# Kernel optimization log

Measured on AMD Instinct MI355X. Metric: run time of the kernel, lower is better.

The kernel has to match this reference:

```python
import jax, jax.numpy as jnp
import numpy as np

N = 20000        # nodes
E = 320000       # edges (avg degree 16)
IN = 128         # in_channels
D = 64           # out_channels == per-head dim (PyG TransformerConv)
H = 4            # heads
EPS_BN = 1e-5


def setup_inputs() -> dict:
    key = jax.random.key(0)
    ks = jax.random.split(key, 12)
    x = jax.random.normal(ks[0], (N, IN), jnp.float32)
    edge_index = jax.random.randint(ks[1], (2, E), 0, N, dtype=jnp.int64)
    s = 1.0 / np.sqrt(IN)
    Wq = jax.random.normal(ks[2], (IN, H * D), jnp.float32) * s
    bq = jnp.zeros((H * D,), jnp.float32)
    Wk = jax.random.normal(ks[3], (IN, H * D), jnp.float32) * s
    bk = jnp.zeros((H * D,), jnp.float32)
    Wv = jax.random.normal(ks[4], (IN, H * D), jnp.float32) * s
    bv = jnp.zeros((H * D,), jnp.float32)
    Wskip = jax.random.normal(ks[5], (IN, D), jnp.float32) * s
    bskip = jnp.zeros((D,), jnp.float32)
    gamma = jnp.ones((D,), jnp.float32)
    beta = jnp.zeros((D,), jnp.float32)
    return {"x": x, "edge_index": edge_index, "Wq": Wq, "bq": bq,
            "Wk": Wk, "bk": bk, "Wv": Wv, "bv": bv,
            "Wskip": Wskip, "bskip": bskip, "gamma": gamma, "beta": beta}


def reference(x, edge_index, Wq, bq, Wk, bk, Wv, bv, Wskip, bskip, gamma, beta):
    src = edge_index[0]   # message source j
    dst = edge_index[1]   # message target i
    # node-level projections, [N, H, D]
    q = (x @ Wq + bq).reshape(N, H, D)
    k = (x @ Wk + bk).reshape(N, H, D)
    v = (x @ Wv + bv).reshape(N, H, D)
    # per-edge attention logits [E, H]
    scores = jnp.einsum('ehd,ehd->eh', q[dst], k[src]) / jnp.sqrt(jnp.float32(D))
    # segment softmax over incoming edges of each target node
    smax = jax.ops.segment_max(scores, dst, num_segments=N)
    smax = jnp.where(jnp.isfinite(smax), smax, 0.0)  # isolated nodes
    p = jnp.exp(scores - smax[dst])
    denom = jax.ops.segment_sum(p, dst, num_segments=N)
    alpha = p / (denom[dst] + 1e-16)                  # [E, H]
    # scatter-aggregate messages: [N, H, D]
    msg = jax.ops.segment_sum(alpha[:, :, None] * v[src], dst, num_segments=N)
    # concat=False -> mean over heads; root skip connection
    out = msg.mean(axis=1) + x @ Wskip + bskip        # [N, D]
    # BatchNorm1d over nodes (training-mode batch stats, biased var)
    mu = out.mean(axis=0)
    var = out.var(axis=0)
    out = (out - mu) * jax.lax.rsqrt(var + EPS_BN) * gamma + beta
    # exact (erf) GELU, dropout = identity at eval
    return jax.nn.gelu(out, approximate=False)
```

## Files before the change

### kernel.cpp

```cpp
#include <hip/hip_runtime.h>
#include <math.h>

#define NNODES 20000
#define NEDGES 320000
#define CIN 128
#define DOUT 64
#define NHEAD 4
#define HD 256
#define PROJW 832

__global__ __launch_bounds__(256) void proj_kernel(
    const float* __restrict__ x,
    const float* __restrict__ Wq, const float* __restrict__ bq,
    const float* __restrict__ Wk, const float* __restrict__ bk,
    const float* __restrict__ Wv, const float* __restrict__ bv,
    const float* __restrict__ Ws, const float* __restrict__ bs,
    float* __restrict__ proj)
{
    __shared__ float Ast[32][68];
    __shared__ float Bs[32][68];
    const int tile_n = blockIdx.x;
    const float* W; const float* bias; int segw; int lc0;
    if (tile_n < 4)       { W = Wq; bias = bq; segw = HD;   lc0 = tile_n * 64; }
    else if (tile_n < 8)  { W = Wk; bias = bk; segw = HD;   lc0 = (tile_n - 4) * 64; }
    else if (tile_n < 12) { W = Wv; bias = bv; segw = HD;   lc0 = (tile_n - 8) * 64; }
    else                  { W = Ws; bias = bs; segw = DOUT; lc0 = 0; }
    const int row0 = blockIdx.y * 64;
    const int tid = threadIdx.x;
    const int tx = tid & 15, ty = tid >> 4;

    float acc[4][4] = {};
    for (int k0 = 0; k0 < CIN; k0 += 32) {
        #pragma unroll
        for (int l = 0; l < 2; ++l) {
            int idx = tid + l * 256;
            int r = idx >> 3, c4 = (idx & 7) << 2;
            int gr = row0 + r;
            float4 v = make_float4(0.f, 0.f, 0.f, 0.f);
            if (gr < NNODES)
                v = *reinterpret_cast<const float4*>(x + (size_t)gr * CIN + k0 + c4);
            Ast[c4 + 0][r] = v.x; Ast[c4 + 1][r] = v.y;
            Ast[c4 + 2][r] = v.z; Ast[c4 + 3][r] = v.w;
        }
        #pragma unroll
        for (int l = 0; l < 2; ++l) {
            int idx = tid + l * 256;
            int r = idx >> 4, c4 = (idx & 15) << 2;
            float4 v = *reinterpret_cast<const float4*>(W + (size_t)(k0 + r) * segw + lc0 + c4);
            *reinterpret_cast<float4*>(&Bs[r][c4]) = v;
        }
        __syncthreads();
        #pragma unroll
        for (int kk = 0; kk < 32; ++kk) {
            const float4 a = *reinterpret_cast<const float4*>(&Ast[kk][ty * 4]);
            const float4 b = *reinterpret_cast<const float4*>(&Bs[kk][tx * 4]);
            acc[0][0] += a.x * b.x; acc[0][1] += a.x * b.y; acc[0][2] += a.x * b.z; acc[0][3] += a.x * b.w;
            acc[1][0] += a.y * b.x; acc[1][1] += a.y * b.y; acc[1][2] += a.y * b.z; acc[1][3] += a.y * b.w;
            acc[2][0] += a.z * b.x; acc[2][1] += a.z * b.y; acc[2][2] += a.z * b.z; acc[2][3] += a.z * b.w;
            acc[3][0] += a.w * b.x; acc[3][1] += a.w * b.y; acc[3][2] += a.w * b.z; acc[3][3] += a.w * b.w;
        }
        __syncthreads();
    }
    const int colg0 = tile_n * 64;
    #pragma unroll
    for (int i = 0; i < 4; ++i) {
        int gr = row0 + ty * 4 + i;
        if (gr < NNODES) {
            float4 o;
            o.x = acc[i][0] + bias[lc0 + tx * 4 + 0];
            o.y = acc[i][1] + bias[lc0 + tx * 4 + 1];
            o.z = acc[i][2] + bias[lc0 + tx * 4 + 2];
            o.w = acc[i][3] + bias[lc0 + tx * 4 + 3];
            *reinterpret_cast<float4*>(proj + (size_t)gr * PROJW + colg0 + tx * 4) = o;
        }
    }
}

__global__ void hist_kernel(const int* __restrict__ ei, int* __restrict__ deg)
{
    int e = blockIdx.x * blockDim.x + threadIdx.x;
    if (e >= NEDGES) return;
    atomicAdd(&deg[ei[NEDGES + e]], 1);
}

__global__ __launch_bounds__(1024) void scan_kernel(
    const int* __restrict__ deg, int* __restrict__ rowptr, int* __restrict__ cursor)
{
    __shared__ int sd[1024];
    const int t = threadIdx.x;
    const int chunk = 20;
    const int base = t * chunk;
    int tsum = 0;
    for (int i = 0; i < chunk; ++i) {
        int idx = base + i;
        tsum += (idx < NNODES) ? deg[idx] : 0;
    }
    sd[t] = tsum; __syncthreads();
    for (int off = 1; off < 1024; off <<= 1) {
        int v = (t >= off) ? sd[t - off] : 0;
        __syncthreads();
        sd[t] += v;
        __syncthreads();
    }
    int run = sd[t] - tsum;
    for (int i = 0; i < chunk; ++i) {
        int idx = base + i;
        if (idx < NNODES) {
            int d = deg[idx];
            rowptr[idx] = run; cursor[idx] = run;
            run += d;
        }
    }
    if (t == 1023) rowptr[NNODES] = sd[1023];
}

__global__ void scatter_kernel(const int* __restrict__ ei, int* __restrict__ cursor,
                               int* __restrict__ col)
{
    int e = blockIdx.x * blockDim.x + threadIdx.x;
    if (e >= NEDGES) return;
    int src = ei[e];
    int dst = ei[NEDGES + e];
    int pos = atomicAdd(&cursor[dst], 1);
    col[pos] = src;
}

__global__ __launch_bounds__(256) void attn_kernel(
    const float* __restrict__ proj,
    const int* __restrict__ rowptr, const int* __restrict__ col,
    float* __restrict__ out_pre)
{
    const int node = blockIdx.x * 4 + (threadIdx.x >> 6);
    if (node >= NNODES) return;
    const int lane = threadIdx.x & 63;
    const int lane4 = lane * 4;

    const size_t nb = (size_t)node * PROJW;
    const float4 q = *reinterpret_cast<const float4*>(proj + nb + lane4);

    float m = -INFINITY, l = 0.f;
    float ax = 0.f, ay = 0.f, az = 0.f, aw = 0.f;
    int p = rowptr[node];
    const int pend = rowptr[node + 1];

    int j = (p < pend) ? col[p] : 0;
    const float* bj = proj + (size_t)j * PROJW + lane4;
    float4 kv = *reinterpret_cast<const float4*>(bj + 256);
    float4 vv = *reinterpret_cast<const float4*>(bj + 512);

    for (; p < pend; ++p) {
        const int p1 = p + 1;
        const int jn = (p1 < pend) ? col[p1] : j;
        const float* bn = proj + (size_t)jn * PROJW + lane4;
        const float4 kvn = *reinterpret_cast<const float4*>(bn + 256);
        const float4 vvn = *reinterpret_cast<const float4*>(bn + 512);

        float partial = q.x * kv.x + q.y * kv.y + q.z * kv.z + q.w * kv.w;
        partial += __shfl_xor(partial, 1, 16);
        partial += __shfl_xor(partial, 2, 16);
        partial += __shfl_xor(partial, 4, 16);
        partial += __shfl_xor(partial, 8, 16);
        const float s = partial * 0.125f;
        const float mnew = fmaxf(m, s);
        const float scale = __expf(m - mnew);
        const float pc = __expf(s - mnew);
        l = l * scale + pc;
        ax = ax * scale + pc * vv.x;
        ay = ay * scale + pc * vv.y;
        az = az * scale + pc * vv.z;
        aw = aw * scale + pc * vv.w;
        m = mnew;
        kv = kvn; vv = vvn;
    }
    const float inv = 1.f / (l + 1e-16f);
    float rx = ax * inv, ry = ay * inv, rz = az * inv, rw = aw * inv;
    rx += __shfl_xor(rx, 16); rx += __shfl_xor(rx, 32);
    ry += __shfl_xor(ry, 16); ry += __shfl_xor(ry, 32);
    rz += __shfl_xor(rz, 16); rz += __shfl_xor(rz, 32);
    rw += __shfl_xor(rw, 16); rw += __shfl_xor(rw, 32);
    if (lane < 16) {
        const float4 sk = *reinterpret_cast<const float4*>(proj + nb + 768 + lane4);
        float4 o;
        o.x = rx * 0.25f + sk.x;
        o.y = ry * 0.25f + sk.y;
        o.z = rz * 0.25f + sk.z;
        o.w = rw * 0.25f + sk.w;
        *reinterpret_cast<float4*>(out_pre + (size_t)node * DOUT + lane4) = o;
    }
}

__global__ __launch_bounds__(256) void bnred_kernel(
    const float* __restrict__ out_pre, float* __restrict__ bnacc)
{
    const int tid = threadIdx.x;
    const int c = tid & 63, g = tid >> 6;
    float s = 0.f, ss = 0.f;
    for (int r = blockIdx.x * 4 + g; r < NNODES; r += gridDim.x * 4) {
        float v = out_pre[(size_t)r * DOUT + c];
        s += v; ss += v * v;
    }
    __shared__ float sd[256];
    sd[tid] = s; __syncthreads();
    float s4 = 0.f;
    if (g == 0) s4 = sd[tid] + sd[tid + 64] + sd[tid + 128] + sd[tid + 192];
    __syncthreads();
    sd[tid] = ss; __syncthreads();
    if (g == 0) {
        float ss4 = sd[tid] + sd[tid + 64] + sd[tid + 128] + sd[tid + 192];
        atomicAdd(&bnacc[c], s4);
        atomicAdd(&bnacc[64 + c], ss4);
    }
}

__global__ __launch_bounds__(256) void final_kernel(
    const float* __restrict__ out_pre, const float* __restrict__ bnacc,
    const float* __restrict__ gamma, const float* __restrict__ beta,
    float* __restrict__ out)
{
    int idx = blockIdx.x * blockDim.x + threadIdx.x;
    if (idx >= NNODES * DOUT) return;
    const int c = idx & 63;
    const float mu = bnacc[c] * (1.f / NNODES);
    const float var = bnacc[64 + c] * (1.f / NNODES) - mu * mu;
    float v = (out_pre[idx] - mu) * rsqrtf(var + 1e-5f) * gamma[c] + beta[c];
    out[idx] = v * 0.5f * (1.f + erff(v * 0.70710678118654752f));
}

extern "C" void kernel_launch(void* const* d_in, const int* in_sizes, int n_in,
                              void* d_out, int out_size, void* d_ws, size_t ws_size,
                              hipStream_t stream) {
    const float* x     = (const float*)d_in[0];
    const int*   ei    = (const int*)d_in[1];
    const float* Wq    = (const float*)d_in[2];
    const float* bq    = (const float*)d_in[3];
    const float* Wk    = (const float*)d_in[4];
    const float* bk    = (const float*)d_in[5];
    const float* Wv    = (const float*)d_in[6];
    const float* bv    = (const float*)d_in[7];
    const float* Wskip = (const float*)d_in[8];
    const float* bskip = (const float*)d_in[9];
    const float* gamma = (const float*)d_in[10];
    const float* beta  = (const float*)d_in[11];
    float* out = (float*)d_out;

    float* proj    = (float*)d_ws;
    float* out_pre = proj + (size_t)NNODES * PROJW;
    float* bnacc   = out_pre + (size_t)NNODES * DOUT;
    int*   deg     = (int*)(bnacc + 128);
    int*   rowptr  = deg + NNODES;
    int*   cursor  = rowptr + NNODES + 1;
    int*   col     = cursor + NNODES;

    hipMemsetAsync(bnacc, 0, (128 + NNODES) * sizeof(int), stream);

    proj_kernel<<<dim3(13, (NNODES + 63) / 64), 256, 0, stream>>>(
        x, Wq, bq, Wk, bk, Wv, bv, Wskip, bskip, proj);
    hist_kernel<<<(NEDGES + 255) / 256, 256, 0, stream>>>(ei, deg);
    scan_kernel<<<1, 1024, 0, stream>>>(deg, rowptr, cursor);
    scatter_kernel<<<(NEDGES + 255) / 256, 256, 0, stream>>>(ei, cursor, col);
    attn_kernel<<<NNODES / 4, 256, 0, stream>>>(proj, rowptr, col, out_pre);
    bnred_kernel<<<128, 256, 0, stream>>>(out_pre, bnacc);
    final_kernel<<<(NNODES * DOUT + 255) / 256, 256, 0, stream>>>(
        out_pre, bnacc, gamma, beta, out);
}
```

Baseline: 316.0 us.

## Store K/V projections in fp16 separate buffer to halve gather traffic

The projection kernel now writes K and V as half precision into a dedicated packed buffer, while Q and the skip projection stay fp32 in a narrower buffer. The attention kernel gathers the per-edge K/V rows as fp16 and converts them to float, halving the bytes moved in the edge gather, which is the dominant random-access cost. It also shrinks the write traffic of the projection. The cost is fp16 rounding of K and V, which adds a small accuracy loss in the attention scores and the aggregation.

After: 277.7 us. 12.1% less time.

```diff
diff --git a/kernel.cpp b/kernel.cpp
--- a/kernel.cpp
+++ b/kernel.cpp
@@ -1,4 +1,5 @@
 #include <hip/hip_runtime.h>
+#include <hip/hip_fp16.h>
 #include <math.h>
 
 #define NNODES 20000
@@ -7,7 +8,8 @@
 #define DOUT 64
 #define NHEAD 4
 #define HD 256
-#define PROJW 832
+#define PROJW 320
+#define KVW 512
 
 __global__ __launch_bounds__(256) void proj_kernel(
     const float* __restrict__ x,
@@ -15,7 +17,7 @@
     const float* __restrict__ Wk, const float* __restrict__ bk,
     const float* __restrict__ Wv, const float* __restrict__ bv,
     const float* __restrict__ Ws, const float* __restrict__ bs,
-    float* __restrict__ proj)
+    float* __restrict__ proj, __half* __restrict__ kvh)
 {
     __shared__ float Ast[32][68];
     __shared__ float Bs[32][68];
@@ -61,17 +63,26 @@
         }
         __syncthreads();
     }
-    const int colg0 = tile_n * 64;
     #pragma unroll
     for (int i = 0; i < 4; ++i) {
         int gr = row0 + ty * 4 + i;
-        if (gr < NNODES) {
-            float4 o;
-            o.x = acc[i][0] + bias[lc0 + tx * 4 + 0];
-            o.y = acc[i][1] + bias[lc0 + tx * 4 + 1];
-            o.z = acc[i][2] + bias[lc0 + tx * 4 + 2];
-            o.w = acc[i][3] + bias[lc0 + tx * 4 + 3];
-            *reinterpret_cast<float4*>(proj + (size_t)gr * PROJW + colg0 + tx * 4) = o;
+        if (gr >= NNODES) continue;
+        float4 o;
+        o.x = acc[i][0] + bias[lc0 + tx * 4 + 0];
+        o.y = acc[i][1] + bias[lc0 + tx * 4 + 1];
+        o.z = acc[i][2] + bias[lc0 + tx * 4 + 2];
+        o.w = acc[i][3] + bias[lc0 + tx * 4 + 3];
+        if (tile_n < 4) {
+            *reinterpret_cast<float4*>(proj + (size_t)gr * PROJW + tile_n * 64 + tx * 4) = o;
+        } else if (tile_n < 12) {
+            int col = (tile_n < 8) ? (tile_n - 4) * 64 + tx * 4
+                                   : 256 + (tile_n - 8) * 64 + tx * 4;
+            __half2 h0 = __floats2half2_rn(o.x, o.y);
+            __half2 h1 = __floats2half2_rn(o.z, o.w);
+            __half2* dst = reinterpret_cast<__half2*>(kvh + (size_t)gr * KVW + col);
+            dst[0] = h0; dst[1] = h1;
+        } else {
+            *reinterpret_cast<float4*>(proj + (size_t)gr * PROJW + 256 + tx * 4) = o;
         }
     }
 }
@@ -126,7 +137,7 @@
 }
 
 __global__ __launch_bounds__(256) void attn_kernel(
-    const float* __restrict__ proj,
+    const float* __restrict__ proj, const __half* __restrict__ kvh,
     const int* __restrict__ rowptr, const int* __restrict__ col,
     float* __restrict__ out_pre)
 {
@@ -135,8 +146,7 @@
     const int lane = threadIdx.x & 63;
     const int lane4 = lane * 4;
 
-    const size_t nb = (size_t)node * PROJW;
-    const float4 q = *reinterpret_cast<const float4*>(proj + nb + lane4);
+    const float4 q = *reinterpret_cast<const float4*>(proj + (size_t)node * PROJW + lane4);
 
     float m = -INFINITY, l = 0.f;
     float ax = 0.f, ay = 0.f, az = 0.f, aw = 0.f;
@@ -144,18 +154,20 @@
     const int pend = rowptr[node + 1];
 
     int j = (p < pend) ? col[p] : 0;
-    const float* bj = proj + (size_t)j * PROJW + lane4;
-    float4 kv = *reinterpret_cast<const float4*>(bj + 256);
-    float4 vv = *reinterpret_cast<const float4*>(bj + 512);
+    const __half* bj = kvh + (size_t)j * KVW + lane4;
+    uint2 kraw = *reinterpret_cast<const uint2*>(bj);
+    uint2 vraw = *reinterpret_cast<const uint2*>(bj + 256);
 
     for (; p < pend; ++p) {
         const int p1 = p + 1;
         const int jn = (p1 < pend) ? col[p1] : j;
-        const float* bn = proj + (size_t)jn * PROJW + lane4;
-        const float4 kvn = *reinterpret_cast<const float4*>(bn + 256);
-        const float4 vvn = *reinterpret_cast<const float4*>(bn + 512);
-
-        float partial = q.x * kv.x + q.y * kv.y + q.z * kv.z + q.w * kv.w;
+        const __half* bn = kvh + (size_t)jn * KVW + lane4;
+        const uint2 krawn = *reinterpret_cast<const uint2*>(bn);
+        const uint2 vrawn = *reinterpret_cast<const uint2*>(bn + 256);
+
+        const float2 k0 = __half22float2(*reinterpret_cast<const __half2*>(&kraw.x));
+        const float2 k1 = __half22float2(*reinterpret_cast<const __half2*>(&kraw.y));
+        float partial = q.x * k0.x + q.y * k0.y + q.z * k1.x + q.w * k1.y;
         partial += __shfl_xor(partial, 1, 16);
         partial += __shfl_xor(partial, 2, 16);
         partial += __shfl_xor(partial, 4, 16);
@@ -164,13 +176,15 @@
         const float mnew = fmaxf(m, s);
         const float scale = __expf(m - mnew);
         const float pc = __expf(s - mnew);
+        const float2 v0 = __half22float2(*reinterpret_cast<const __half2*>(&vraw.x));
+        const float2 v1 = __half22float2(*reinterpret_cast<const __half2*>(&vraw.y));
         l = l * scale + pc;
-        ax = ax * scale + pc * vv.x;
-        ay = ay * scale + pc * vv.y;
-        az = az * scale + pc * vv.z;
-        aw = aw * scale + pc * vv.w;
+        ax = ax * scale + pc * v0.x;
+        ay = ay * scale + pc * v0.y;
+        az = az * scale + pc * v1.x;
+        aw = aw * scale + pc * v1.y;
         m = mnew;
-        kv = kvn; vv = vvn;
+        kraw = krawn; vraw = vrawn;
     }
     const float inv = 1.f / (l + 1e-16f);
     float rx = ax * inv, ry = ay * inv, rz = az * inv, rw = aw * inv;
@@ -179,7 +193,7 @@
     rz += __shfl_xor(rz, 16); rz += __shfl_xor(rz, 32);
     rw += __shfl_xor(rw, 16); rw += __shfl_xor(rw, 32);
     if (lane < 16) {
-        const float4 sk = *reinterpret_cast<const float4*>(proj + nb + 768 + lane4);
+        const float4 sk = *reinterpret_cast<const float4*>(proj + (size_t)node * PROJW + 256 + lane4);
         float4 o;
         o.x = rx * 0.25f + sk.x;
         o.y = ry * 0.25f + sk.y;
@@ -243,22 +257,23 @@
     const float* beta  = (const float*)d_in[11];
     float* out = (float*)d_out;
 
-    float* proj    = (float*)d_ws;
-    float* out_pre = proj + (size_t)NNODES * PROJW;
-    float* bnacc   = out_pre + (size_t)NNODES * DOUT;
-    int*   deg     = (int*)(bnacc + 128);
-    int*   rowptr  = deg + NNODES;
-    int*   cursor  = rowptr + NNODES + 1;
-    int*   col     = cursor + NNODES;
+    __half* kvh     = (__half*)d_ws;
+    float*  proj    = (float*)((char*)d_ws + (size_t)NNODES * KVW * sizeof(__half));
+    float*  out_pre = proj + (size_t)NNODES * PROJW;
+    float*  bnacc   = out_pre + (size_t)NNODES * DOUT;
+    int*    deg     = (int*)(bnacc + 128);
+    int*    rowptr  = deg + NNODES;
+    int*    cursor  = rowptr + NNODES + 1;
+    int*    col     = cursor + NNODES;
 
     hipMemsetAsync(bnacc, 0, (128 + NNODES) * sizeof(int), stream);
 
     proj_kernel<<<dim3(13, (NNODES + 63) / 64), 256, 0, stream>>>(
-        x, Wq, bq, Wk, bk, Wv, bv, Wskip, bskip, proj);
+        x, Wq, bq, Wk, bk, Wv, bv, Wskip, bskip, proj, kvh);
     hist_kernel<<<(NEDGES + 255) / 256, 256, 0, stream>>>(ei, deg);
     scan_kernel<<<1, 1024, 0, stream>>>(deg, rowptr, cursor);
     scatter_kernel<<<(NEDGES + 255) / 256, 256, 0, stream>>>(ei, cursor, col);
-    attn_kernel<<<NNODES / 4, 256, 0, stream>>>(proj, rowptr, col, out_pre);
+    attn_kernel<<<NNODES / 4, 256, 0, stream>>>(proj, kvh, rowptr, col, out_pre);
     bnred_kernel<<<128, 256, 0, stream>>>(out_pre, bnacc);
     final_kernel<<<(NNODES * DOUT + 255) / 256, 256, 0, stream>>>(
         out_pre, bnacc, gamma, beta, out);
```
